# Kernel tuning notes

Measured on AMD Instinct MI355X. Metric: run time of the kernel, lower is better.

Reference implementation:

```python
import jax, jax.numpy as jnp
import numpy as np
import math

HEAD_NUM = 32
D_K = 128
HIDDEN = 4096
MAX_BS = 16
MAX_SEQ = 2048


def setup_inputs() -> dict:
    key = jax.random.key(0)
    ks = jax.random.split(key, 7)
    s = 1.0 / math.sqrt(HIDDEN)
    return {
        "x": jax.random.normal(ks[0], (MAX_BS, 1, HIDDEN), dtype=jnp.float32),
        "cache_k": jax.random.normal(ks[1], (MAX_BS, MAX_SEQ, HEAD_NUM, D_K), dtype=jnp.float32),
        "cache_v": jax.random.normal(ks[2], (MAX_BS, MAX_SEQ, HEAD_NUM, D_K), dtype=jnp.float32),
        "w_q": jax.random.normal(ks[3], (HIDDEN, HIDDEN), dtype=jnp.float32) * s,
        "w_k": jax.random.normal(ks[4], (HIDDEN, HIDDEN), dtype=jnp.float32) * s,
        "w_v": jax.random.normal(ks[5], (HIDDEN, HIDDEN), dtype=jnp.float32) * s,
        "w_o": jax.random.normal(ks[6], (HIDDEN, HIDDEN), dtype=jnp.float32) * s,
        "start_pos": 2047,
    }


def reference(x, cache_k, cache_v, w_q, w_k, w_v, w_o, start_pos):
    B, S, H = x.shape  # S == 1 (single decode token, per the module's .view(..., 1, ...))
    # QKV projections (bias-free linears)
    q = (x @ w_q).reshape(B, S, HEAD_NUM, D_K)
    k = (x @ w_k).reshape(B, S, HEAD_NUM, D_K)
    v = (x @ w_v).reshape(B, S, HEAD_NUM, D_K)
    # Write the new token into the KV cache at start_pos
    cache_k = jax.lax.dynamic_update_slice(cache_k, k, (0, start_pos, 0, 0))
    cache_v = jax.lax.dynamic_update_slice(cache_v, v, (0, start_pos, 0, 0))
    # Attend over the valid prefix [0, start_pos + S)
    keys = cache_k[:B, : start_pos + S]    # [B, T, H, D]
    values = cache_v[:B, : start_pos + S]  # [B, T, H, D]
    scale = 1.0 / math.sqrt(D_K)
    scores = jnp.einsum("bqhd,bkhd->bhqk", q, keys) * scale  # [B, H, S, T]
    attn = jax.nn.softmax(scores, axis=-1)
    out = jnp.einsum("bhqk,bkhd->bqhd", attn, values)  # [B, S, H, D]
    out = out.reshape(B, S, H * 0 + HEAD_NUM * D_K)
    return out @ w_o
```

## Files before the change

### kernel.cpp

```cpp
#include <hip/hip_runtime.h>

#define HEAD_NUM 32
#define D_K 128
#define HIDDEN 4096
#define MAX_BS 16
#define MAX_SEQ 2048
#define NCHUNK 8
#define CHUNK 256

__global__ __launch_bounds__(256) void qkv_kernel(
    const float* __restrict__ x,
    const float* __restrict__ w_q,
    const float* __restrict__ w_k,
    const float* __restrict__ w_v,
    float* __restrict__ qkv)
{
    __shared__ float xs[MAX_BS][128];
    const int colTile = blockIdx.x;
    const int kChunk  = blockIdx.y;
    const int mat     = blockIdx.z;
    const int tid     = threadIdx.x;

    const float* W = (mat == 0) ? w_q : (mat == 1) ? w_k : w_v;
    float* outp = qkv + (size_t)mat * (MAX_BS * HIDDEN);

    for (int idx = tid; idx < MAX_BS * 128 / 4; idx += 256) {
        int b = idx >> 5;
        int f = idx & 31;
        *reinterpret_cast<float4*>(&xs[b][f * 4]) =
            *reinterpret_cast<const float4*>(&x[b * HIDDEN + kChunk * 128 + f * 4]);
    }
    __syncthreads();

    const int col = colTile * 256 + tid;
    float acc[MAX_BS];
    #pragma unroll
    for (int b = 0; b < MAX_BS; ++b) acc[b] = 0.f;

    const float* wcol = W + (size_t)(kChunk * 128) * HIDDEN + col;
    #pragma unroll 4
    for (int ii = 0; ii < 128; ++ii) {
        float w = wcol[(size_t)ii * HIDDEN];
        #pragma unroll
        for (int b = 0; b < MAX_BS; ++b)
            acc[b] = fmaf(xs[b][ii], w, acc[b]);
    }

    #pragma unroll
    for (int b = 0; b < MAX_BS; ++b)
        atomicAdd(&outp[b * HIDDEN + col], acc[b]);
}

__global__ __launch_bounds__(256) void attn_partial_kernel(
    const float* __restrict__ cache_k,
    const float* __restrict__ cache_v,
    const float* __restrict__ qkv,
    const int*   __restrict__ start_pos_p,
    float* __restrict__ part_o,
    float* __restrict__ part_ml)
{
    const int h   = blockIdx.x;
    const int b   = blockIdx.y;
    const int c   = blockIdx.z;
    const int tid = threadIdx.x;
    const int start_pos = *start_pos_p;
    const int seq_len   = start_pos + 1;
    const int s0        = c * CHUNK;

    __shared__ float sc[CHUNK];
    __shared__ float red[8];
    __shared__ float partial[8][D_K];

    const float* q    = qkv + b * HIDDEN + h * D_K;
    const float* knew = qkv + 1 * (MAX_BS * HIDDEN) + b * HIDDEN + h * D_K;
    const float* vnew = qkv + 2 * (MAX_BS * HIDDEN) + b * HIDDEN + h * D_K;

    const int lane32 = tid & 31;
    const int grp    = tid >> 5;
    const int wid    = tid >> 6;

    const float4 qf = *reinterpret_cast<const float4*>(&q[lane32 * 4]);
    const float scale = 0.08838834764831845f;

    sc[tid] = -INFINITY;
    __syncthreads();

    for (int r = grp; r < CHUNK; r += 8) {
        const int s = s0 + r;
        if (s >= seq_len) break;
        const float* krow = (s == start_pos)
            ? knew
            : cache_k + (((size_t)b * MAX_SEQ + s) * HEAD_NUM + h) * D_K;
        const float4 kf = *reinterpret_cast<const float4*>(&krow[lane32 * 4]);
        float p = qf.x * kf.x + qf.y * kf.y + qf.z * kf.z + qf.w * kf.w;
        p += __shfl_xor(p, 16);
        p += __shfl_xor(p, 8);
        p += __shfl_xor(p, 4);
        p += __shfl_xor(p, 2);
        p += __shfl_xor(p, 1);
        if (lane32 == 0) sc[r] = p * scale;
    }
    __syncthreads();

    float m = sc[tid];
    #pragma unroll
    for (int off = 32; off; off >>= 1) m = fmaxf(m, __shfl_xor(m, off));
    if ((tid & 63) == 0) red[wid] = m;
    __syncthreads();
    m = fmaxf(fmaxf(red[0], red[1]), fmaxf(red[2], red[3]));

    const float raw = sc[tid];
    const float e = (raw == -INFINITY) ? 0.f : __expf(raw - m);
    sc[tid] = e;
    float sum = e;
    #pragma unroll
    for (int off = 32; off; off >>= 1) sum += __shfl_xor(sum, off);
    if ((tid & 63) == 0) red[4 + wid] = sum;
    __syncthreads();
    sum = red[4] + red[5] + red[6] + red[7];

    float4 accv = {0.f, 0.f, 0.f, 0.f};
    for (int r = grp; r < CHUNK; r += 8) {
        const int s = s0 + r;
        if (s >= seq_len) break;
        const float* vrow = (s == start_pos)
            ? vnew
            : cache_v + (((size_t)b * MAX_SEQ + s) * HEAD_NUM + h) * D_K;
        const float4 vf = *reinterpret_cast<const float4*>(&vrow[lane32 * 4]);
        const float p = sc[r];
        accv.x = fmaf(p, vf.x, accv.x);
        accv.y = fmaf(p, vf.y, accv.y);
        accv.z = fmaf(p, vf.z, accv.z);
        accv.w = fmaf(p, vf.w, accv.w);
    }
    *reinterpret_cast<float4*>(&partial[grp][lane32 * 4]) = accv;
    __syncthreads();

    const size_t base = (size_t)(b * HEAD_NUM + h) * NCHUNK + c;
    if (tid < D_K) {
        float r = 0.f;
        #pragma unroll
        for (int g = 0; g < 8; ++g) r += partial[g][tid];
        part_o[base * D_K + tid] = r;
    }
    if (tid == 0) {
        part_ml[base * 2 + 0] = m;
        part_ml[base * 2 + 1] = sum;
    }
}

__global__ __launch_bounds__(128) void attn_combine_kernel(
    const float* __restrict__ part_o,
    const float* __restrict__ part_ml,
    float* __restrict__ attn_out)
{
    const int h   = blockIdx.x;
    const int b   = blockIdx.y;
    const int tid = threadIdx.x;
    const size_t base = (size_t)(b * HEAD_NUM + h) * NCHUNK;

    float mv[NCHUNK];
    float M = -INFINITY;
    #pragma unroll
    for (int c = 0; c < NCHUNK; ++c) {
        mv[c] = part_ml[(base + c) * 2];
        M = fmaxf(M, mv[c]);
    }
    float acc = 0.f, l = 0.f;
    #pragma unroll
    for (int c = 0; c < NCHUNK; ++c) {
        const float w = __expf(mv[c] - M);
        acc += w * part_o[(base + c) * D_K + tid];
        l   += w * part_ml[(base + c) * 2 + 1];
    }
    attn_out[b * HIDDEN + h * D_K + tid] = acc / l;
}

__global__ __launch_bounds__(256) void oproj_kernel(
    const float* __restrict__ attn_out,
    const float* __restrict__ w_o,
    float* __restrict__ out)
{
    __shared__ float xs[MAX_BS][128];
    const int colTile = blockIdx.x;
    const int kChunk  = blockIdx.y;
    const int tid     = threadIdx.x;

    for (int idx = tid; idx < MAX_BS * 128 / 4; idx += 256) {
        int b = idx >> 5;
        int f = idx & 31;
        *reinterpret_cast<float4*>(&xs[b][f * 4]) =
            *reinterpret_cast<const float4*>(&attn_out[b * HIDDEN + kChunk * 128 + f * 4]);
    }
    __syncthreads();

    const int col = colTile * 256 + tid;
    float acc[MAX_BS];
    #pragma unroll
    for (int b = 0; b < MAX_BS; ++b) acc[b] = 0.f;

    const float* wcol = w_o + (size_t)(kChunk * 128) * HIDDEN + col;
    #pragma unroll 4
    for (int ii = 0; ii < 128; ++ii) {
        float w = wcol[(size_t)ii * HIDDEN];
        #pragma unroll
        for (int b = 0; b < MAX_BS; ++b)
            acc[b] = fmaf(xs[b][ii], w, acc[b]);
    }

    #pragma unroll
    for (int b = 0; b < MAX_BS; ++b)
        atomicAdd(&out[b * HIDDEN + col], acc[b]);
}

extern "C" void kernel_launch(void* const* d_in, const int* in_sizes, int n_in,
                              void* d_out, int out_size, void* d_ws, size_t ws_size,
                              hipStream_t stream) {
    const float* x       = (const float*)d_in[0];
    const float* cache_k = (const float*)d_in[1];
    const float* cache_v = (const float*)d_in[2];
    const float* w_q     = (const float*)d_in[3];
    const float* w_k     = (const float*)d_in[4];
    const float* w_v     = (const float*)d_in[5];
    const float* w_o     = (const float*)d_in[6];
    const int*   start_pos = (const int*)d_in[7];

    float* out      = (float*)d_out;
    float* qkv      = (float*)d_ws;
    float* attn_out = qkv + 3 * MAX_BS * HIDDEN;
    float* part_o   = attn_out + MAX_BS * HIDDEN;
    float* part_ml  = part_o + (size_t)MAX_BS * HEAD_NUM * NCHUNK * D_K;

    hipMemsetAsync(qkv, 0, (size_t)3 * MAX_BS * HIDDEN * sizeof(float), stream);
    hipMemsetAsync(d_out, 0, (size_t)out_size * sizeof(float), stream);

    qkv_kernel<<<dim3(16, 32, 3), 256, 0, stream>>>(x, w_q, w_k, w_v, qkv);
    attn_partial_kernel<<<dim3(HEAD_NUM, MAX_BS, NCHUNK), 256, 0, stream>>>(
        cache_k, cache_v, qkv, start_pos, part_o, part_ml);
    attn_combine_kernel<<<dim3(HEAD_NUM, MAX_BS), 128, 0, stream>>>(
        part_o, part_ml, attn_out);
    oproj_kernel<<<dim3(16, 32), 256, 0, stream>>>(attn_out, w_o, out);
}
```

Baseline: 269.0 us.

## Overlap K/V projection with cached attention and fold new token into combine

The Q projection now runs in its own kernel with a finer k-split. The K/V projections are merged into a single launch with the cache-prefix attention blocks, so their weight streaming overlaps with the KV-cache reads. The attention blocks now skip the new token, and the combine kernel adds its score and value as an extra softmax term. This removes the dependency of attention on K/V projection, at the cost of a heterogeneous grid and a larger shared-memory footprint for attention blocks.

```diff
diff --git a/kernel.cpp b/kernel.cpp
--- a/kernel.cpp
+++ b/kernel.cpp
@@ -7,160 +7,205 @@
 #define MAX_SEQ 2048
 #define NCHUNK 8
 #define CHUNK 256
-
-__global__ __launch_bounds__(256) void qkv_kernel(
+#define NATTN (HEAD_NUM * MAX_BS * NCHUNK)
+#define NKV   (16 * 32 * 2)
+
+__global__ __launch_bounds__(256) void qproj_kernel(
     const float* __restrict__ x,
     const float* __restrict__ w_q,
+    float* __restrict__ qbuf)
+{
+    __shared__ float xs[MAX_BS][64];
+    const int colTile = blockIdx.x;
+    const int kChunk  = blockIdx.y;
+    const int tid     = threadIdx.x;
+
+    {
+        int b = tid >> 4;
+        int f = tid & 15;
+        *reinterpret_cast<float4*>(&xs[b][f * 4]) =
+            *reinterpret_cast<const float4*>(&x[b * HIDDEN + kChunk * 64 + f * 4]);
+    }
+    __syncthreads();
+
+    const int col = colTile * 256 + tid;
+    float acc[MAX_BS];
+    #pragma unroll
+    for (int b = 0; b < MAX_BS; ++b) acc[b] = 0.f;
+
+    const float* wcol = w_q + (size_t)(kChunk * 64) * HIDDEN + col;
+    #pragma unroll 4
+    for (int ii = 0; ii < 64; ++ii) {
+        float w = wcol[(size_t)ii * HIDDEN];
+        #pragma unroll
+        for (int b = 0; b < MAX_BS; ++b)
+            acc[b] = fmaf(xs[b][ii], w, acc[b]);
+    }
+
+    #pragma unroll
+    for (int b = 0; b < MAX_BS; ++b)
+        atomicAdd(&qbuf[b * HIDDEN + col], acc[b]);
+}
+
+__global__ __launch_bounds__(256) void fused_attn_kv_kernel(
+    const float* __restrict__ x,
     const float* __restrict__ w_k,
     const float* __restrict__ w_v,
-    float* __restrict__ qkv)
-{
-    __shared__ float xs[MAX_BS][128];
-    const int colTile = blockIdx.x;
-    const int kChunk  = blockIdx.y;
-    const int mat     = blockIdx.z;
-    const int tid     = threadIdx.x;
-
-    const float* W = (mat == 0) ? w_q : (mat == 1) ? w_k : w_v;
-    float* outp = qkv + (size_t)mat * (MAX_BS * HIDDEN);
-
-    for (int idx = tid; idx < MAX_BS * 128 / 4; idx += 256) {
-        int b = idx >> 5;
-        int f = idx & 31;
-        *reinterpret_cast<float4*>(&xs[b][f * 4]) =
-            *reinterpret_cast<const float4*>(&x[b * HIDDEN + kChunk * 128 + f * 4]);
-    }
-    __syncthreads();
-
-    const int col = colTile * 256 + tid;
-    float acc[MAX_BS];
-    #pragma unroll
-    for (int b = 0; b < MAX_BS; ++b) acc[b] = 0.f;
-
-    const float* wcol = W + (size_t)(kChunk * 128) * HIDDEN + col;
-    #pragma unroll 4
-    for (int ii = 0; ii < 128; ++ii) {
-        float w = wcol[(size_t)ii * HIDDEN];
-        #pragma unroll
-        for (int b = 0; b < MAX_BS; ++b)
-            acc[b] = fmaf(xs[b][ii], w, acc[b]);
-    }
-
-    #pragma unroll
-    for (int b = 0; b < MAX_BS; ++b)
-        atomicAdd(&outp[b * HIDDEN + col], acc[b]);
-}
-
-__global__ __launch_bounds__(256) void attn_partial_kernel(
     const float* __restrict__ cache_k,
     const float* __restrict__ cache_v,
-    const float* __restrict__ qkv,
+    float* __restrict__ qkv,
     const int*   __restrict__ start_pos_p,
     float* __restrict__ part_o,
     float* __restrict__ part_ml)
 {
+    __shared__ float smem[MAX_BS * 128];
+    const int bid = blockIdx.x;
+    const int tid = threadIdx.x;
+
+    if (bid < NATTN) {
+        float* sc  = smem;
+        float* red = smem + 256;
+        float (*partial)[D_K] = reinterpret_cast<float(*)[D_K]>(smem + 264);
+
+        const int c = bid & 7;
+        const int b = (bid >> 3) & 15;
+        const int h = bid >> 7;
+        const int start_pos = *start_pos_p;
+        const int s0 = c * CHUNK;
+
+        const float* q = qkv + b * HIDDEN + h * D_K;
+        const int lane32 = tid & 31;
+        const int grp    = tid >> 5;
+        const int wid    = tid >> 6;
+
+        const float4 qf = *reinterpret_cast<const float4*>(&q[lane32 * 4]);
+        const float scale = 0.08838834764831845f;
+
+        sc[tid] = -INFINITY;
+        __syncthreads();
+
+        for (int r = grp; r < CHUNK; r += 8) {
+            const int s = s0 + r;
+            if (s >= start_pos) break;
+            const float* krow = cache_k + (((size_t)b * MAX_SEQ + s) * HEAD_NUM + h) * D_K;
+            const float4 kf = *reinterpret_cast<const float4*>(&krow[lane32 * 4]);
+            float p = qf.x * kf.x + qf.y * kf.y + qf.z * kf.z + qf.w * kf.w;
+            p += __shfl_xor(p, 16);
+            p += __shfl_xor(p, 8);
+            p += __shfl_xor(p, 4);
+            p += __shfl_xor(p, 2);
+            p += __shfl_xor(p, 1);
+            if (lane32 == 0) sc[r] = p * scale;
+        }
+        __syncthreads();
+
+        float m = sc[tid];
+        #pragma unroll
+        for (int off = 32; off; off >>= 1) m = fmaxf(m, __shfl_xor(m, off));
+        if ((tid & 63) == 0) red[wid] = m;
+        __syncthreads();
+        m = fmaxf(fmaxf(red[0], red[1]), fmaxf(red[2], red[3]));
+
+        const float raw = sc[tid];
+        const float e = (raw == -INFINITY) ? 0.f : __expf(raw - m);
+        __syncthreads();
+        sc[tid] = e;
+        float sum = e;
+        #pragma unroll
+        for (int off = 32; off; off >>= 1) sum += __shfl_xor(sum, off);
+        if ((tid & 63) == 0) red[4 + wid] = sum;
+        __syncthreads();
+        sum = red[4] + red[5] + red[6] + red[7];
+
+        float4 accv = {0.f, 0.f, 0.f, 0.f};
+        for (int r = grp; r < CHUNK; r += 8) {
+            const int s = s0 + r;
+            if (s >= start_pos) break;
+            const float* vrow = cache_v + (((size_t)b * MAX_SEQ + s) * HEAD_NUM + h) * D_K;
+            const float4 vf = *reinterpret_cast<const float4*>(&vrow[lane32 * 4]);
+            const float p = sc[r];
+            accv.x = fmaf(p, vf.x, accv.x);
+            accv.y = fmaf(p, vf.y, accv.y);
+            accv.z = fmaf(p, vf.z, accv.z);
+            accv.w = fmaf(p, vf.w, accv.w);
+        }
+        *reinterpret_cast<float4*>(&partial[grp][lane32 * 4]) = accv;
+        __syncthreads();
+
+        const size_t base = (size_t)(b * HEAD_NUM + h) * NCHUNK + c;
+        if (tid < D_K) {
+            float r = 0.f;
+            #pragma unroll
+            for (int g = 0; g < 8; ++g) r += partial[g][tid];
+            part_o[base * D_K + tid] = r;
+        }
+        if (tid == 0) {
+            part_ml[base * 2 + 0] = m;
+            part_ml[base * 2 + 1] = sum;
+        }
+    } else {
+        float (*xs)[128] = reinterpret_cast<float(*)[128]>(smem);
+        const int t       = bid - NATTN;
+        const int colTile = t & 15;
+        const int kChunk  = (t >> 4) & 31;
+        const int mat     = 1 + (t >> 9);
+
+        const float* W = (mat == 1) ? w_k : w_v;
+        float* outp = qkv + (size_t)mat * (MAX_BS * HIDDEN);
+
+        for (int idx = tid; idx < MAX_BS * 128 / 4; idx += 256) {
+            int b = idx >> 5;
+            int f = idx & 31;
+            *reinterpret_cast<float4*>(&xs[b][f * 4]) =
+                *reinterpret_cast<const float4*>(&x[b * HIDDEN + kChunk * 128 + f * 4]);
+        }
+        __syncthreads();
+
+        const int col = colTile * 256 + tid;
+        float acc[MAX_BS];
+        #pragma unroll
+        for (int b = 0; b < MAX_BS; ++b) acc[b] = 0.f;
+
+        const float* wcol = W + (size_t)(kChunk * 128) * HIDDEN + col;
+        #pragma unroll 4
+        for (int ii = 0; ii < 128; ++ii) {
+            float w = wcol[(size_t)ii * HIDDEN];
+            #pragma unroll
+            for (int b = 0; b < MAX_BS; ++b)
+                acc[b] = fmaf(xs[b][ii], w, acc[b]);
+        }
+
+        #pragma unroll
+        for (int b = 0; b < MAX_BS; ++b)
+            atomicAdd(&outp[b * HIDDEN + col], acc[b]);
+    }
+}
+
+__global__ __launch_bounds__(128) void combine_kernel(
+    const float* __restrict__ qkv,
+    const float* __restrict__ part_o,
+    const float* __restrict__ part_ml,
+    float* __restrict__ attn_out)
+{
     const int h   = blockIdx.x;
     const int b   = blockIdx.y;
-    const int c   = blockIdx.z;
     const int tid = threadIdx.x;
-    const int start_pos = *start_pos_p;
-    const int seq_len   = start_pos + 1;
-    const int s0        = c * CHUNK;
-
-    __shared__ float sc[CHUNK];
-    __shared__ float red[8];
-    __shared__ float partial[8][D_K];
+    __shared__ float redS[2];
 
     const float* q    = qkv + b * HIDDEN + h * D_K;
     const float* knew = qkv + 1 * (MAX_BS * HIDDEN) + b * HIDDEN + h * D_K;
     const float* vnew = qkv + 2 * (MAX_BS * HIDDEN) + b * HIDDEN + h * D_K;
 
-    const int lane32 = tid & 31;
-    const int grp    = tid >> 5;
-    const int wid    = tid >> 6;
-
-    const float4 qf = *reinterpret_cast<const float4*>(&q[lane32 * 4]);
-    const float scale = 0.08838834764831845f;
-
-    sc[tid] = -INFINITY;
+    float pp = q[tid] * knew[tid];
+    #pragma unroll
+    for (int off = 32; off; off >>= 1) pp += __shfl_xor(pp, off);
+    if ((tid & 63) == 0) redS[tid >> 6] = pp;
     __syncthreads();
-
-    for (int r = grp; r < CHUNK; r += 8) {
-        const int s = s0 + r;
-        if (s >= seq_len) break;
-        const float* krow = (s == start_pos)
-            ? knew
-            : cache_k + (((size_t)b * MAX_SEQ + s) * HEAD_NUM + h) * D_K;
-        const float4 kf = *reinterpret_cast<const float4*>(&krow[lane32 * 4]);
-        float p = qf.x * kf.x + qf.y * kf.y + qf.z * kf.z + qf.w * kf.w;
-        p += __shfl_xor(p, 16);
-        p += __shfl_xor(p, 8);
-        p += __shfl_xor(p, 4);
-        p += __shfl_xor(p, 2);
-        p += __shfl_xor(p, 1);
-        if (lane32 == 0) sc[r] = p * scale;
-    }
-    __syncthreads();
-
-    float m = sc[tid];
-    #pragma unroll
-    for (int off = 32; off; off >>= 1) m = fmaxf(m, __shfl_xor(m, off));
-    if ((tid & 63) == 0) red[wid] = m;
-    __syncthreads();
-    m = fmaxf(fmaxf(red[0], red[1]), fmaxf(red[2], red[3]));
-
-    const float raw = sc[tid];
-    const float e = (raw == -INFINITY) ? 0.f : __expf(raw - m);
-    sc[tid] = e;
-    float sum = e;
-    #pragma unroll
-    for (int off = 32; off; off >>= 1) sum += __shfl_xor(sum, off);
-    if ((tid & 63) == 0) red[4 + wid] = sum;
-    __syncthreads();
-    sum = red[4] + red[5] + red[6] + red[7];
-
-    float4 accv = {0.f, 0.f, 0.f, 0.f};
-    for (int r = grp; r < CHUNK; r += 8) {
-        const int s = s0 + r;
-        if (s >= seq_len) break;
-        const float* vrow = (s == start_pos)
-            ? vnew
-            : cache_v + (((size_t)b * MAX_SEQ + s) * HEAD_NUM + h) * D_K;
-        const float4 vf = *reinterpret_cast<const float4*>(&vrow[lane32 * 4]);
-        const float p = sc[r];
-        accv.x = fmaf(p, vf.x, accv.x);
-        accv.y = fmaf(p, vf.y, accv.y);
-        accv.z = fmaf(p, vf.z, accv.z);
-        accv.w = fmaf(p, vf.w, accv.w);
-    }
-    *reinterpret_cast<float4*>(&partial[grp][lane32 * 4]) = accv;
-    __syncthreads();
-
-    const size_t base = (size_t)(b * HEAD_NUM + h) * NCHUNK + c;
-    if (tid < D_K) {
-        float r = 0.f;
-        #pragma unroll
-        for (int g = 0; g < 8; ++g) r += partial[g][tid];
-        part_o[base * D_K + tid] = r;
-    }
-    if (tid == 0) {
-        part_ml[base * 2 + 0] = m;
-        part_ml[base * 2 + 1] = sum;
-    }
-}
-
-__global__ __launch_bounds__(128) void attn_combine_kernel(
-    const float* __restrict__ part_o,
-    const float* __restrict__ part_ml,
-    float* __restrict__ attn_out)
-{
-    const int h   = blockIdx.x;
-    const int b   = blockIdx.y;
-    const int tid = threadIdx.x;
+    const float score = (redS[0] + redS[1]) * 0.08838834764831845f;
+
     const size_t base = (size_t)(b * HEAD_NUM + h) * NCHUNK;
-
     float mv[NCHUNK];
-    float M = -INFINITY;
+    float M = score;
     #pragma unroll
     for (int c = 0; c < NCHUNK; ++c) {
         mv[c] = part_ml[(base + c) * 2];
@@ -173,6 +218,10 @@
         acc += w * part_o[(base + c) * D_K + tid];
         l   += w * part_ml[(base + c) * 2 + 1];
     }
+    const float wn = __expf(score - M);
+    acc += wn * vnew[tid];
+    l   += wn;
+
     attn_out[b * HIDDEN + h * D_K + tid] = acc / l;
 }
 
@@ -234,10 +283,10 @@
     hipMemsetAsync(qkv, 0, (size_t)3 * MAX_BS * HIDDEN * sizeof(float), stream);
     hipMemsetAsync(d_out, 0, (size_t)out_size * sizeof(float), stream);
 
-    qkv_kernel<<<dim3(16, 32, 3), 256, 0, stream>>>(x, w_q, w_k, w_v, qkv);
-    attn_partial_kernel<<<dim3(HEAD_NUM, MAX_BS, NCHUNK), 256, 0, stream>>>(
-        cache_k, cache_v, qkv, start_pos, part_o, part_ml);
-    attn_combine_kernel<<<dim3(HEAD_NUM, MAX_BS), 128, 0, stream>>>(
-        part_o, part_ml, attn_out);
+    qproj_kernel<<<dim3(16, 64), 256, 0, stream>>>(x, w_q, qkv);
+    fused_attn_kv_kernel<<<dim3(NATTN + NKV), 256, 0, stream>>>(
+        x, w_k, w_v, cache_k, cache_v, qkv, start_pos, part_o, part_ml);
+    combine_kernel<<<dim3(HEAD_NUM, MAX_BS), 128, 0, stream>>>(
+        qkv, part_o, part_ml, attn_out);
     oproj_kernel<<<dim3(16, 32), 256, 0, stream>>>(attn_out, w_o, out);
 }
```

Result: slower. 315.0 us (+17.1%).

## Replace atomic split-K with partial buffers and fold new token into combine

Applied to the files above, without the earlier changes.

The QKV and output projection GEMVs now write per-split partial sums to workspace, and separate reduce kernels sum them. This removes float atomics and the two memsets. The new token's key/value contribution is moved out of the attention partial kernel into the combine step, so the partial loops read only cache rows with unrolled, branch-free indexing. The cost is extra workspace traffic: a 32-way partial buffer for each of the four matrices must be written and read back, plus two more kernel launches.

```diff
diff --git a/kernel.cpp b/kernel.cpp
--- a/kernel.cpp
+++ b/kernel.cpp
@@ -7,13 +7,14 @@
 #define MAX_SEQ 2048
 #define NCHUNK 8
 #define CHUNK 256
-
-__global__ __launch_bounds__(256) void qkv_kernel(
+#define NSPLIT 32
+
+__global__ __launch_bounds__(256) void qkv_gemv_kernel(
     const float* __restrict__ x,
     const float* __restrict__ w_q,
     const float* __restrict__ w_k,
     const float* __restrict__ w_v,
-    float* __restrict__ qkv)
+    float* __restrict__ partials)
 {
     __shared__ float xs[MAX_BS][128];
     const int colTile = blockIdx.x;
@@ -22,7 +23,6 @@
     const int tid     = threadIdx.x;
 
     const float* W = (mat == 0) ? w_q : (mat == 1) ? w_k : w_v;
-    float* outp = qkv + (size_t)mat * (MAX_BS * HIDDEN);
 
     for (int idx = tid; idx < MAX_BS * 128 / 4; idx += 256) {
         int b = idx >> 5;
@@ -46,9 +46,25 @@
             acc[b] = fmaf(xs[b][ii], w, acc[b]);
     }
 
+    float* outp = partials + ((size_t)(mat * NSPLIT + kChunk) * MAX_BS) * HIDDEN + col;
     #pragma unroll
     for (int b = 0; b < MAX_BS; ++b)
-        atomicAdd(&outp[b * HIDDEN + col], acc[b]);
+        outp[(size_t)b * HIDDEN] = acc[b];
+}
+
+__global__ __launch_bounds__(256) void qkv_reduce_kernel(
+    const float* __restrict__ partials,
+    float* __restrict__ qkv)
+{
+    const int idx = blockIdx.x * 256 + threadIdx.x;
+    const int mat = idx / (MAX_BS * HIDDEN);
+    const int rem = idx - mat * (MAX_BS * HIDDEN);
+    const float* p = partials + (size_t)mat * NSPLIT * MAX_BS * HIDDEN + rem;
+    float s = 0.f;
+    #pragma unroll
+    for (int c = 0; c < NSPLIT; ++c)
+        s += p[(size_t)c * MAX_BS * HIDDEN];
+    qkv[idx] = s;
 }
 
 __global__ __launch_bounds__(256) void attn_partial_kernel(
@@ -64,17 +80,15 @@
     const int c   = blockIdx.z;
     const int tid = threadIdx.x;
     const int start_pos = *start_pos_p;
-    const int seq_len   = start_pos + 1;
     const int s0        = c * CHUNK;
+    int nrows = start_pos - s0;
+    nrows = (nrows < 0) ? 0 : (nrows > CHUNK ? CHUNK : nrows);
 
     __shared__ float sc[CHUNK];
     __shared__ float red[8];
     __shared__ float partial[8][D_K];
 
-    const float* q    = qkv + b * HIDDEN + h * D_K;
-    const float* knew = qkv + 1 * (MAX_BS * HIDDEN) + b * HIDDEN + h * D_K;
-    const float* vnew = qkv + 2 * (MAX_BS * HIDDEN) + b * HIDDEN + h * D_K;
-
+    const float* q = qkv + b * HIDDEN + h * D_K;
     const int lane32 = tid & 31;
     const int grp    = tid >> 5;
     const int wid    = tid >> 6;
@@ -85,13 +99,11 @@
     sc[tid] = -INFINITY;
     __syncthreads();
 
-    for (int r = grp; r < CHUNK; r += 8) {
-        const int s = s0 + r;
-        if (s >= seq_len) break;
-        const float* krow = (s == start_pos)
-            ? knew
-            : cache_k + (((size_t)b * MAX_SEQ + s) * HEAD_NUM + h) * D_K;
-        const float4 kf = *reinterpret_cast<const float4*>(&krow[lane32 * 4]);
+    const float* kbase = cache_k + (((size_t)b * MAX_SEQ + s0) * HEAD_NUM + h) * D_K;
+    #pragma unroll 4
+    for (int r = grp; r < nrows; r += 8) {
+        const float4 kf = *reinterpret_cast<const float4*>(
+            &kbase[(size_t)r * (HEAD_NUM * D_K) + lane32 * 4]);
         float p = qf.x * kf.x + qf.y * kf.y + qf.z * kf.z + qf.w * kf.w;
         p += __shfl_xor(p, 16);
         p += __shfl_xor(p, 8);
@@ -111,6 +123,7 @@
 
     const float raw = sc[tid];
     const float e = (raw == -INFINITY) ? 0.f : __expf(raw - m);
+    __syncthreads();
     sc[tid] = e;
     float sum = e;
     #pragma unroll
@@ -120,13 +133,11 @@
     sum = red[4] + red[5] + red[6] + red[7];
 
     float4 accv = {0.f, 0.f, 0.f, 0.f};
-    for (int r = grp; r < CHUNK; r += 8) {
-        const int s = s0 + r;
-        if (s >= seq_len) break;
-        const float* vrow = (s == start_pos)
-            ? vnew
-            : cache_v + (((size_t)b * MAX_SEQ + s) * HEAD_NUM + h) * D_K;
-        const float4 vf = *reinterpret_cast<const float4*>(&vrow[lane32 * 4]);
+    const float* vbase = cache_v + (((size_t)b * MAX_SEQ + s0) * HEAD_NUM + h) * D_K;
+    #pragma unroll 4
+    for (int r = grp; r < nrows; r += 8) {
+        const float4 vf = *reinterpret_cast<const float4*>(
+            &vbase[(size_t)r * (HEAD_NUM * D_K) + lane32 * 4]);
         const float p = sc[r];
         accv.x = fmaf(p, vf.x, accv.x);
         accv.y = fmaf(p, vf.y, accv.y);
@@ -149,7 +160,8 @@
     }
 }
 
-__global__ __launch_bounds__(128) void attn_combine_kernel(
+__global__ __launch_bounds__(128) void combine_kernel(
+    const float* __restrict__ qkv,
     const float* __restrict__ part_o,
     const float* __restrict__ part_ml,
     float* __restrict__ attn_out)
@@ -157,10 +169,22 @@
     const int h   = blockIdx.x;
     const int b   = blockIdx.y;
     const int tid = threadIdx.x;
+    __shared__ float redS[2];
+
+    const float* q    = qkv + b * HIDDEN + h * D_K;
+    const float* knew = qkv + 1 * (MAX_BS * HIDDEN) + b * HIDDEN + h * D_K;
+    const float* vnew = qkv + 2 * (MAX_BS * HIDDEN) + b * HIDDEN + h * D_K;
+
+    float pp = q[tid] * knew[tid];
+    #pragma unroll
+    for (int off = 32; off; off >>= 1) pp += __shfl_xor(pp, off);
+    if ((tid & 63) == 0) redS[tid >> 6] = pp;
+    __syncthreads();
+    const float score = (redS[0] + redS[1]) * 0.08838834764831845f;
+
     const size_t base = (size_t)(b * HEAD_NUM + h) * NCHUNK;
-
     float mv[NCHUNK];
-    float M = -INFINITY;
+    float M = score;
     #pragma unroll
     for (int c = 0; c < NCHUNK; ++c) {
         mv[c] = part_ml[(base + c) * 2];
@@ -173,13 +197,17 @@
         acc += w * part_o[(base + c) * D_K + tid];
         l   += w * part_ml[(base + c) * 2 + 1];
     }
+    const float wn = __expf(score - M);
+    acc += wn * vnew[tid];
+    l   += wn;
+
     attn_out[b * HIDDEN + h * D_K + tid] = acc / l;
 }
 
-__global__ __launch_bounds__(256) void oproj_kernel(
+__global__ __launch_bounds__(256) void oproj_gemv_kernel(
     const float* __restrict__ attn_out,
     const float* __restrict__ w_o,
-    float* __restrict__ out)
+    float* __restrict__ partials)
 {
     __shared__ float xs[MAX_BS][128];
     const int colTile = blockIdx.x;
@@ -208,9 +236,23 @@
             acc[b] = fmaf(xs[b][ii], w, acc[b]);
     }
 
+    float* outp = partials + (size_t)kChunk * MAX_BS * HIDDEN + col;
     #pragma unroll
     for (int b = 0; b < MAX_BS; ++b)
-        atomicAdd(&out[b * HIDDEN + col], acc[b]);
+        outp[(size_t)b * HIDDEN] = acc[b];
+}
+
+__global__ __launch_bounds__(256) void oproj_reduce_kernel(
+    const float* __restrict__ partials,
+    float* __restrict__ out)
+{
+    const int idx = blockIdx.x * 256 + threadIdx.x;
+    const float* p = partials + idx;
+    float s = 0.f;
+    #pragma unroll
+    for (int c = 0; c < NSPLIT; ++c)
+        s += p[(size_t)c * MAX_BS * HIDDEN];
+    out[idx] = s;
 }
 
 extern "C" void kernel_launch(void* const* d_in, const int* in_sizes, int n_in,
@@ -230,14 +272,15 @@
     float* attn_out = qkv + 3 * MAX_BS * HIDDEN;
     float* part_o   = attn_out + MAX_BS * HIDDEN;
     float* part_ml  = part_o + (size_t)MAX_BS * HEAD_NUM * NCHUNK * D_K;
-
-    hipMemsetAsync(qkv, 0, (size_t)3 * MAX_BS * HIDDEN * sizeof(float), stream);
-    hipMemsetAsync(d_out, 0, (size_t)out_size * sizeof(float), stream);
-
-    qkv_kernel<<<dim3(16, 32, 3), 256, 0, stream>>>(x, w_q, w_k, w_v, qkv);
+    float* pq       = part_ml + (size_t)MAX_BS * HEAD_NUM * NCHUNK * 2;
+    float* po       = pq + (size_t)3 * NSPLIT * MAX_BS * HIDDEN;
+
+    qkv_gemv_kernel<<<dim3(16, NSPLIT, 3), 256, 0, stream>>>(x, w_q, w_k, w_v, pq);
+    qkv_reduce_kernel<<<dim3(3 * MAX_BS * HIDDEN / 256), 256, 0, stream>>>(pq, qkv);
     attn_partial_kernel<<<dim3(HEAD_NUM, MAX_BS, NCHUNK), 256, 0, stream>>>(
         cache_k, cache_v, qkv, start_pos, part_o, part_ml);
-    attn_combine_kernel<<<dim3(HEAD_NUM, MAX_BS), 128, 0, stream>>>(
-        part_o, part_ml, attn_out);
-    oproj_kernel<<<dim3(16, 32), 256, 0, stream>>>(attn_out, w_o, out);
-}
+    combine_kernel<<<dim3(HEAD_NUM, MAX_BS), 128, 0, stream>>>(
+        qkv, part_o, part_ml, attn_out);
+    oproj_gemv_kernel<<<dim3(16, NSPLIT), 256, 0, stream>>>(attn_out, w_o, po);
+    oproj_reduce_kernel<<<dim3(MAX_BS * HIDDEN / 256), 256, 0, stream>>>(po, out);
+}
```

After: 285.2 us. 6.0% more time.

## Fold new-token attention into combine kernel and widen KV loads in partial kernel

Applied to the files above, without the earlier changes.

The new token's score and value are now computed in the combine kernel as an extra softmax term, taken straight from the QKV workspace. This removes the per-row start_pos branch and early-exit checks from the partial kernel, which now runs a fixed 16-iteration unrolled loop over its whole chunk. Each row is read by 16 lanes with two float4 loads each, so more memory requests are in flight. The trade-off is that the stale cache row at start_pos and any rows beyond the valid length are still loaded and then masked. A barrier is also added before the shared score buffer is overwritten, which closes a read/write race.

```diff
diff --git a/kernel.cpp b/kernel.cpp
--- a/kernel.cpp
+++ b/kernel.cpp
@@ -64,41 +64,39 @@
     const int c   = blockIdx.z;
     const int tid = threadIdx.x;
     const int start_pos = *start_pos_p;
-    const int seq_len   = start_pos + 1;
     const int s0        = c * CHUNK;
 
     __shared__ float sc[CHUNK];
     __shared__ float red[8];
-    __shared__ float partial[8][D_K];
-
-    const float* q    = qkv + b * HIDDEN + h * D_K;
-    const float* knew = qkv + 1 * (MAX_BS * HIDDEN) + b * HIDDEN + h * D_K;
-    const float* vnew = qkv + 2 * (MAX_BS * HIDDEN) + b * HIDDEN + h * D_K;
-
-    const int lane32 = tid & 31;
-    const int grp    = tid >> 5;
+    __shared__ float partial[16][D_K];
+
+    const int lane16 = tid & 15;
+    const int grp    = tid >> 4;
     const int wid    = tid >> 6;
 
-    const float4 qf = *reinterpret_cast<const float4*>(&q[lane32 * 4]);
+    const float* q = qkv + b * HIDDEN + h * D_K;
+    const float4 q0 = *reinterpret_cast<const float4*>(&q[lane16 * 8]);
+    const float4 q1 = *reinterpret_cast<const float4*>(&q[lane16 * 8 + 4]);
     const float scale = 0.08838834764831845f;
 
-    sc[tid] = -INFINITY;
-    __syncthreads();
-
-    for (int r = grp; r < CHUNK; r += 8) {
-        const int s = s0 + r;
-        if (s >= seq_len) break;
-        const float* krow = (s == start_pos)
-            ? knew
-            : cache_k + (((size_t)b * MAX_SEQ + s) * HEAD_NUM + h) * D_K;
-        const float4 kf = *reinterpret_cast<const float4*>(&krow[lane32 * 4]);
-        float p = qf.x * kf.x + qf.y * kf.y + qf.z * kf.z + qf.w * kf.w;
-        p += __shfl_xor(p, 16);
+    const size_t rowstride = (size_t)HEAD_NUM * D_K;
+    const float* kbase = cache_k + (((size_t)b * MAX_SEQ + s0) * HEAD_NUM + h) * D_K;
+    const float* vbase = cache_v + (((size_t)b * MAX_SEQ + s0) * HEAD_NUM + h) * D_K;
+
+    #pragma unroll 4
+    for (int it = 0; it < 16; ++it) {
+        const int r = it * 16 + grp;
+        const float* krow = kbase + (size_t)r * rowstride + lane16 * 8;
+        const float4 k0 = *reinterpret_cast<const float4*>(krow);
+        const float4 k1 = *reinterpret_cast<const float4*>(krow + 4);
+        float p = q0.x * k0.x + q0.y * k0.y + q0.z * k0.z + q0.w * k0.w
+                + q1.x * k1.x + q1.y * k1.y + q1.z * k1.z + q1.w * k1.w;
         p += __shfl_xor(p, 8);
         p += __shfl_xor(p, 4);
         p += __shfl_xor(p, 2);
         p += __shfl_xor(p, 1);
-        if (lane32 == 0) sc[r] = p * scale;
+        if (lane16 == 0)
+            sc[r] = (s0 + r < start_pos) ? p * scale : -INFINITY;
     }
     __syncthreads();
 
@@ -111,6 +109,7 @@
 
     const float raw = sc[tid];
     const float e = (raw == -INFINITY) ? 0.f : __expf(raw - m);
+    __syncthreads();
     sc[tid] = e;
     float sum = e;
     #pragma unroll
@@ -119,28 +118,29 @@
     __syncthreads();
     sum = red[4] + red[5] + red[6] + red[7];
 
-    float4 accv = {0.f, 0.f, 0.f, 0.f};
-    for (int r = grp; r < CHUNK; r += 8) {
-        const int s = s0 + r;
-        if (s >= seq_len) break;
-        const float* vrow = (s == start_pos)
-            ? vnew
-            : cache_v + (((size_t)b * MAX_SEQ + s) * HEAD_NUM + h) * D_K;
-        const float4 vf = *reinterpret_cast<const float4*>(&vrow[lane32 * 4]);
+    float4 a0 = {0.f, 0.f, 0.f, 0.f};
+    float4 a1 = {0.f, 0.f, 0.f, 0.f};
+    #pragma unroll 4
+    for (int it = 0; it < 16; ++it) {
+        const int r = it * 16 + grp;
+        const float* vrow = vbase + (size_t)r * rowstride + lane16 * 8;
+        const float4 v0 = *reinterpret_cast<const float4*>(vrow);
+        const float4 v1 = *reinterpret_cast<const float4*>(vrow + 4);
         const float p = sc[r];
-        accv.x = fmaf(p, vf.x, accv.x);
-        accv.y = fmaf(p, vf.y, accv.y);
-        accv.z = fmaf(p, vf.z, accv.z);
-        accv.w = fmaf(p, vf.w, accv.w);
-    }
-    *reinterpret_cast<float4*>(&partial[grp][lane32 * 4]) = accv;
+        a0.x = fmaf(p, v0.x, a0.x);  a0.y = fmaf(p, v0.y, a0.y);
+        a0.z = fmaf(p, v0.z, a0.z);  a0.w = fmaf(p, v0.w, a0.w);
+        a1.x = fmaf(p, v1.x, a1.x);  a1.y = fmaf(p, v1.y, a1.y);
+        a1.z = fmaf(p, v1.z, a1.z);  a1.w = fmaf(p, v1.w, a1.w);
+    }
+    *reinterpret_cast<float4*>(&partial[grp][lane16 * 8])     = a0;
+    *reinterpret_cast<float4*>(&partial[grp][lane16 * 8 + 4]) = a1;
     __syncthreads();
 
     const size_t base = (size_t)(b * HEAD_NUM + h) * NCHUNK + c;
     if (tid < D_K) {
         float r = 0.f;
         #pragma unroll
-        for (int g = 0; g < 8; ++g) r += partial[g][tid];
+        for (int g = 0; g < 16; ++g) r += partial[g][tid];
         part_o[base * D_K + tid] = r;
     }
     if (tid == 0) {
@@ -149,7 +149,8 @@
     }
 }
 
-__global__ __launch_bounds__(128) void attn_combine_kernel(
+__global__ __launch_bounds__(128) void combine_kernel(
+    const float* __restrict__ qkv,
     const float* __restrict__ part_o,
     const float* __restrict__ part_ml,
     float* __restrict__ attn_out)
@@ -157,10 +158,22 @@
     const int h   = blockIdx.x;
     const int b   = blockIdx.y;
     const int tid = threadIdx.x;
+    __shared__ float redS[2];
+
+    const float* q    = qkv + b * HIDDEN + h * D_K;
+    const float* knew = qkv + 1 * (MAX_BS * HIDDEN) + b * HIDDEN + h * D_K;
+    const float* vnew = qkv + 2 * (MAX_BS * HIDDEN) + b * HIDDEN + h * D_K;
+
+    float pp = q[tid] * knew[tid];
+    #pragma unroll
+    for (int off = 32; off; off >>= 1) pp += __shfl_xor(pp, off);
+    if ((tid & 63) == 0) redS[tid >> 6] = pp;
+    __syncthreads();
+    const float score = (redS[0] + redS[1]) * 0.08838834764831845f;
+
     const size_t base = (size_t)(b * HEAD_NUM + h) * NCHUNK;
-
     float mv[NCHUNK];
-    float M = -INFINITY;
+    float M = score;
     #pragma unroll
     for (int c = 0; c < NCHUNK; ++c) {
         mv[c] = part_ml[(base + c) * 2];
@@ -173,6 +186,10 @@
         acc += w * part_o[(base + c) * D_K + tid];
         l   += w * part_ml[(base + c) * 2 + 1];
     }
+    const float wn = __expf(score - M);
+    acc += wn * vnew[tid];
+    l   += wn;
+
     attn_out[b * HIDDEN + h * D_K + tid] = acc / l;
 }
 
@@ -237,7 +254,7 @@
     qkv_kernel<<<dim3(16, 32, 3), 256, 0, stream>>>(x, w_q, w_k, w_v, qkv);
     attn_partial_kernel<<<dim3(HEAD_NUM, MAX_BS, NCHUNK), 256, 0, stream>>>(
         cache_k, cache_v, qkv, start_pos, part_o, part_ml);
-    attn_combine_kernel<<<dim3(HEAD_NUM, MAX_BS), 128, 0, stream>>>(
-        part_o, part_ml, attn_out);
+    combine_kernel<<<dim3(HEAD_NUM, MAX_BS), 128, 0, stream>>>(
+        qkv, part_o, part_ml, attn_out);
     oproj_kernel<<<dim3(16, 32), 256, 0, stream>>>(attn_out, w_o, out);
 }
```

After: 275.0 us. +2.2%, slower.
